# Kernel optimization log

Measured on AMD Instinct MI355X. Metric: run time of the kernel, lower is better.

The kernel has to match this reference:

```python
import jax, jax.numpy as jnp
import numpy as np

H = 4096          # hidden_size
I = 14336         # intermediate_size
SC = int(0.3 * I) # beta * I -> size of cached x_topk (4300)
HC = int(0.05 * I)# gamma * I -> helper top-k count (716)


def setup_inputs() -> dict:
    key = jax.random.key(0)
    ks = jax.random.split(key, 7)
    s = 0.02
    return {
        "x": jax.random.normal(ks[0], (1, 1, H), dtype=jnp.float32),
        "x_topk": jax.random.randint(ks[1], (SC,), 0, I, dtype=jnp.int64),
        "gate_w": jax.random.normal(ks[2], (I, H), dtype=jnp.float32) * s,
        "up_w": jax.random.normal(ks[3], (I, H), dtype=jnp.float32) * s,
        "down_w": jax.random.normal(ks[4], (H, I), dtype=jnp.float32) * s,
        "helper_w1": jax.random.normal(ks[5], (1024, H), dtype=jnp.float32) * s,
        "helper_w2": jax.random.normal(ks[6], (I, 1024), dtype=jnp.float32) * s,
    }


def reference(x, x_topk, gate_w, up_w, down_w, helper_w1, helper_w2):
    # --- sparsity predictor (SimpleLinearModel): two bias-free linears ---
    h = (x @ helper_w1.T) @ helper_w2.T                       # [1,1,I]
    up_mask_index = jax.lax.top_k(h.reshape(-1), HC)[1]       # [HC]

    # --- combine cached core indices with predicted indices, dedup ---
    combined = jnp.concatenate([x_topk.astype(jnp.int32),
                                up_mask_index.astype(jnp.int32)])  # [SC+HC]
    K = combined.shape[0]
    uniq = jnp.unique(combined, size=K, fill_value=I)         # padded with I
    valid = (uniq < I)                                        # [K] bool
    idx = jnp.where(valid, uniq, 0)                           # safe gather idx

    # --- gather weight rows/columns, reduced gated-MLP matmul ---
    gate_f = gate_w[idx]                                      # [K,H]
    up_f = up_w[idx]                                          # [K,H]
    gate_out = jnp.einsum('bsh,kh->bsk', x, gate_f)           # [1,1,K]
    up_out = jnp.einsum('bsh,kh->bsk', x, up_f)               # [1,1,K]
    tv = jax.nn.silu(gate_out) * up_out                       # act_fn = SiLU
    tv = tv * valid.astype(tv.dtype)                          # zero padded dups

    down_f = down_w[:, idx]                                   # [H,K]
    down_value = jnp.einsum('bsk,hk->bsh', tv, down_f)        # [1,1,H]
    return down_value
```

## Files before the change

### kernel.cpp

```cpp
#include <hip/hip_runtime.h>
#include <math.h>

#define H_DIM 4096
#define I_DIM 14336
#define HB_DIM 1024
#define SC_K 4300
#define HC_K 716

__device__ __forceinline__ unsigned sortable(float f) {
    unsigned u = __float_as_uint(f);
    return (u & 0x80000000u) ? ~u : (u | 0x80000000u);
}

__device__ __forceinline__ void compute_tv_row(const float* __restrict__ x,
                                               const float* __restrict__ gate_w,
                                               const float* __restrict__ up_w,
                                               float* __restrict__ tv, int row, int lane) {
    const float* gr = gate_w + (size_t)row * H_DIM;
    const float* ur = up_w + (size_t)row * H_DIM;
    float gs = 0.f, us = 0.f;
#pragma unroll 4
    for (int c = 0; c < H_DIM; c += 256) {
        int cc = c + lane * 4;
        float4 xv = *(const float4*)(x + cc);
        float4 g = *(const float4*)(gr + cc);
        float4 u = *(const float4*)(ur + cc);
        gs += g.x * xv.x + g.y * xv.y + g.z * xv.z + g.w * xv.w;
        us += u.x * xv.x + u.y * xv.y + u.z * xv.z + u.w * xv.w;
    }
#pragma unroll
    for (int o = 32; o >= 1; o >>= 1) {
        gs += __shfl_xor(gs, o);
        us += __shfl_xor(us, o);
    }
    if (lane == 0) {
        float s = gs / (1.f + expf(-gs));
        tv[row] = s * us;
    }
}

__global__ __launch_bounds__(256) void k1_h1_gateup(
    const float* __restrict__ x, const float* __restrict__ hw1,
    const int* __restrict__ x_topk, const float* __restrict__ gate_w,
    const float* __restrict__ up_w, float* __restrict__ h1,
    float* __restrict__ tv) {
    int wid = threadIdx.x >> 6, lane = threadIdx.x & 63;
    int b = blockIdx.x;
    if (b < 256) {
        int row = b * 4 + wid;
        const float* mr = hw1 + (size_t)row * H_DIM;
        float s = 0.f;
#pragma unroll 4
        for (int c = 0; c < H_DIM; c += 256) {
            int cc = c + lane * 4;
            float4 m = *(const float4*)(mr + cc);
            float4 v = *(const float4*)(x + cc);
            s += m.x * v.x + m.y * v.y + m.z * v.z + m.w * v.w;
        }
#pragma unroll
        for (int o = 32; o >= 1; o >>= 1) s += __shfl_xor(s, o);
        if (lane == 0) h1[row] = s;
    } else {
        int gw = (b - 256) * 4 + wid;
        if (gw < SC_K) {
            int idx = x_topk[gw];
            if ((unsigned)idx < (unsigned)I_DIM)
                compute_tv_row(x, gate_w, up_w, tv, idx, lane);
        }
    }
}

__global__ __launch_bounds__(256) void k2_h(
    const float* __restrict__ h1, const float* __restrict__ hw2,
    float* __restrict__ hbuf) {
    int wid = threadIdx.x >> 6, lane = threadIdx.x & 63;
    int row = blockIdx.x * 4 + wid;
    const float* mr = hw2 + (size_t)row * HB_DIM;
    float s = 0.f;
#pragma unroll
    for (int c = 0; c < HB_DIM; c += 256) {
        int cc = c + lane * 4;
        float4 m = *(const float4*)(mr + cc);
        float4 v = *(const float4*)(h1 + cc);
        s += m.x * v.x + m.y * v.y + m.z * v.z + m.w * v.w;
    }
#pragma unroll
    for (int o = 32; o >= 1; o >>= 1) s += __shfl_xor(s, o);
    if (lane == 0) hbuf[row] = s;
}

__global__ __launch_bounds__(1024) void select_kernel(
    const float* __restrict__ h, const int* __restrict__ x_topk,
    float* __restrict__ tv, int* __restrict__ rlist, int* __restrict__ rcount) {
    __shared__ unsigned bins[2048];
    __shared__ unsigned wpart[16];
    __shared__ unsigned bitT[448], bitS[448];
    __shared__ int s_b, s_above, s_tie_cnt, s_rc;
    __shared__ int tie_idx[2048];
    int tid = threadIdx.x;
    int lane = tid & 63, wid = tid >> 6;

    unsigned key[14];
#pragma unroll
    for (int j = 0; j < 14; ++j) key[j] = sortable(h[j * 1024 + tid]);

    if (tid < 448) { bitT[tid] = 0; bitS[tid] = 0; }
    if (tid == 0) { s_tie_cnt = 0; s_rc = 0; }
    __syncthreads();

    for (int k = tid; k < SC_K; k += 1024) {
        int idx = x_topk[k];
        if ((unsigned)idx < (unsigned)I_DIM) atomicOr(&bitT[idx >> 5], 1u << (idx & 31));
    }

    int b1 = 0, b2 = 0;
    int above = 0;
    unsigned T = 0;
    int need2 = 0;

    for (int pass = 0; pass < 3; ++pass) {
        int nb = (pass == 2) ? 1024 : 2048;
        bins[tid] = 0;
        if (nb == 2048) bins[tid + 1024] = 0;
        __syncthreads();
#pragma unroll
        for (int j = 0; j < 14; ++j) {
            unsigned u = key[j];
            bool in_sub = (pass == 0) ||
                          ((pass == 1) ? ((int)(u >> 21) == b1)
                                       : ((int)(u >> 21) == b1 && (int)((u >> 10) & 0x7FF) == b2));
            if (in_sub) {
                unsigned k = (pass == 0) ? (u >> 21)
                           : (pass == 1) ? ((u >> 10) & 0x7FF)
                                         : (u & 0x3FF);
                atomicAdd(&bins[k], 1u);
            }
        }
        __syncthreads();
        unsigned c0 = (2 * tid < nb) ? bins[2 * tid] : 0u;
        unsigned c1 = (2 * tid + 1 < nb) ? bins[2 * tid + 1] : 0u;
        unsigned s = c0 + c1;
        unsigned incl = s;
#pragma unroll
        for (int o = 1; o < 64; o <<= 1) {
            unsigned v = __shfl_up(incl, o);
            if (lane >= o) incl += v;
        }
        if (lane == 63) wpart[wid] = incl;
        __syncthreads();
        if (wid == 0 && lane < 16) {
            unsigned p = wpart[lane];
#pragma unroll
            for (int o = 1; o < 16; o <<= 1) {
                unsigned v = __shfl_up(p, o, 16);
                if (lane >= o) p += v;
            }
            wpart[lane] = p;
        }
        __syncthreads();
        unsigned total = wpart[15];
        unsigned base = (wid > 0 ? wpart[wid - 1] : 0u) + (incl - s);
        unsigned need = (unsigned)(HC_K - above);
        if (2 * tid < nb) {
            unsigned Pm1 = base, P = base + c0;
            if (total - P < need && total - Pm1 >= need) { s_b = 2 * tid; s_above = above + (int)(total - P); }
        }
        if (2 * tid + 1 < nb) {
            unsigned Pm1 = base + c0, P = base + c0 + c1;
            if (total - P < need && total - Pm1 >= need) { s_b = 2 * tid + 1; s_above = above + (int)(total - P); }
        }
        __syncthreads();
        if (pass == 0) b1 = s_b;
        else if (pass == 1) b2 = s_b;
        above = s_above;
        if (pass == 2) {
            T = ((unsigned)b1 << 21) | ((unsigned)b2 << 10) | (unsigned)s_b;
            need2 = HC_K - above;
        }
        __syncthreads();
    }

#pragma unroll
    for (int j = 0; j < 14; ++j) {
        unsigned u = key[j];
        int i = j * 1024 + tid;
        if (u > T) atomicOr(&bitS[i >> 5], 1u << (i & 31));
        else if (u == T) {
            int p = atomicAdd(&s_tie_cnt, 1);
            if (p < 2048) tie_idx[p] = i;
        }
    }
    __syncthreads();
    int C = s_tie_cnt;
    if (C <= 2048) {
        for (int m = tid; m < C; m += 1024) {
            int my = tie_idx[m];
            int rank = 0;
            for (int j = 0; j < C; ++j) rank += (tie_idx[j] < my) ? 1 : 0;
            if (rank < need2) atomicOr(&bitS[my >> 5], 1u << (my & 31));
        }
    } else if (tid == 0) {
        int left = need2;
        for (int i = 0; i < I_DIM && left > 0; ++i)
            if (sortable(h[i]) == T) { atomicOr(&bitS[i >> 5], 1u << (i & 31)); --left; }
    }
    __syncthreads();

#pragma unroll
    for (int j = 0; j < 14; ++j) {
        int i = j * 1024 + tid;
        bool t = (bitT[i >> 5] >> (i & 31)) & 1u;
        bool sl = (bitS[i >> 5] >> (i & 31)) & 1u;
        if (!t) {
            if (sl) {
                int p = atomicAdd(&s_rc, 1);
                rlist[p] = i;
            } else {
                tv[i] = 0.f;
            }
        }
    }
    __syncthreads();
    if (tid == 0) *rcount = s_rc;
}

__global__ __launch_bounds__(256) void k3_residual(
    const float* __restrict__ x, const float* __restrict__ gate_w,
    const float* __restrict__ up_w, const int* __restrict__ rlist,
    const int* __restrict__ rcount, float* __restrict__ tv) {
    int wid = threadIdx.x >> 6, lane = threadIdx.x & 63;
    int gw = blockIdx.x * 4 + wid;
    if (gw < *rcount) compute_tv_row(x, gate_w, up_w, tv, rlist[gw], lane);
}

__global__ __launch_bounds__(256) void k4_down(
    const float* __restrict__ tv, const float* __restrict__ down_w,
    float* __restrict__ out) {
    int wid = threadIdx.x >> 6, lane = threadIdx.x & 63;
    int row = blockIdx.x * 4 + wid;
    const float* mr = down_w + (size_t)row * I_DIM;
    float s = 0.f;
#pragma unroll 4
    for (int c = 0; c < I_DIM; c += 256) {
        int cc = c + lane * 4;
        float4 m = *(const float4*)(mr + cc);
        float4 v = *(const float4*)(tv + cc);
        s += m.x * v.x + m.y * v.y + m.z * v.z + m.w * v.w;
    }
#pragma unroll
    for (int o = 32; o >= 1; o >>= 1) s += __shfl_xor(s, o);
    if (lane == 0) out[row] = s;
}

extern "C" void kernel_launch(void* const* d_in, const int* in_sizes, int n_in,
                              void* d_out, int out_size, void* d_ws, size_t ws_size,
                              hipStream_t stream) {
    const float* x      = (const float*)d_in[0];
    const int*   x_topk = (const int*)d_in[1];
    const float* gate_w = (const float*)d_in[2];
    const float* up_w   = (const float*)d_in[3];
    const float* down_w = (const float*)d_in[4];
    const float* hw1    = (const float*)d_in[5];
    const float* hw2    = (const float*)d_in[6];
    float* out = (float*)d_out;

    float* ws    = (float*)d_ws;
    float* h1    = ws;
    float* hbuf  = ws + 1024;
    float* tv    = ws + 1024 + I_DIM;
    int*   rlist = (int*)(ws + 1024 + 2 * I_DIM);
    int*   rcount = rlist + 768;

    k1_h1_gateup<<<256 + (SC_K + 3) / 4, 256, 0, stream>>>(x, hw1, x_topk, gate_w,
                                                           up_w, h1, tv);
    k2_h<<<I_DIM / 4, 256, 0, stream>>>(h1, hw2, hbuf);
    select_kernel<<<1, 1024, 0, stream>>>(hbuf, x_topk, tv, rlist, rcount);
    k3_residual<<<(HC_K + 3) / 4, 256, 0, stream>>>(x, gate_w, up_w, rlist, rcount, tv);
    k4_down<<<H_DIM / 4, 256, 0, stream>>>(tv, down_w, out);
}
```

Before: 103.7 us.

## Fuse top-k selection with residual gate/up rows, replicating selection per block

The single-block select kernel and the residual gate/up kernel are merged into one kernel launched with 256 blocks. Each block redundantly recomputes the full top-k selection, then handles its own 56-row slice, zeroing unselected tv entries and computing tv for selected rows not already in the cached set. This removes one launch, the rlist/rcount round trip through global memory and the atomic compaction. In exchange every block repeats the radix selection, and the residual rows can be unevenly spread across blocks.

```diff
diff --git a/kernel.cpp b/kernel.cpp
--- a/kernel.cpp
+++ b/kernel.cpp
@@ -89,13 +89,14 @@
     if (lane == 0) hbuf[row] = s;
 }
 
-__global__ __launch_bounds__(1024) void select_kernel(
+__global__ __launch_bounds__(1024) void k3_select_residual(
     const float* __restrict__ h, const int* __restrict__ x_topk,
-    float* __restrict__ tv, int* __restrict__ rlist, int* __restrict__ rcount) {
+    const float* __restrict__ x, const float* __restrict__ gate_w,
+    const float* __restrict__ up_w, float* __restrict__ tv) {
     __shared__ unsigned bins[2048];
     __shared__ unsigned wpart[16];
     __shared__ unsigned bitT[448], bitS[448];
-    __shared__ int s_b, s_above, s_tie_cnt, s_rc;
+    __shared__ int s_b, s_above, s_tie_cnt;
     __shared__ int tie_idx[2048];
     int tid = threadIdx.x;
     int lane = tid & 63, wid = tid >> 6;
@@ -105,7 +106,7 @@
     for (int j = 0; j < 14; ++j) key[j] = sortable(h[j * 1024 + tid]);
 
     if (tid < 448) { bitT[tid] = 0; bitS[tid] = 0; }
-    if (tid == 0) { s_tie_cnt = 0; s_rc = 0; }
+    if (tid == 0) s_tie_cnt = 0;
     __syncthreads();
 
     for (int k = tid; k < SC_K; k += 1024) {
@@ -206,31 +207,19 @@
     }
     __syncthreads();
 
-#pragma unroll
-    for (int j = 0; j < 14; ++j) {
-        int i = j * 1024 + tid;
+    int base_row = blockIdx.x * 56;
+    for (int r = tid; r < 56; r += 1024) {
+        int i = base_row + r;
         bool t = (bitT[i >> 5] >> (i & 31)) & 1u;
         bool sl = (bitS[i >> 5] >> (i & 31)) & 1u;
-        if (!t) {
-            if (sl) {
-                int p = atomicAdd(&s_rc, 1);
-                rlist[p] = i;
-            } else {
-                tv[i] = 0.f;
-            }
-        }
-    }
-    __syncthreads();
-    if (tid == 0) *rcount = s_rc;
-}
-
-__global__ __launch_bounds__(256) void k3_residual(
-    const float* __restrict__ x, const float* __restrict__ gate_w,
-    const float* __restrict__ up_w, const int* __restrict__ rlist,
-    const int* __restrict__ rcount, float* __restrict__ tv) {
-    int wid = threadIdx.x >> 6, lane = threadIdx.x & 63;
-    int gw = blockIdx.x * 4 + wid;
-    if (gw < *rcount) compute_tv_row(x, gate_w, up_w, tv, rlist[gw], lane);
+        if (!t && !sl) tv[i] = 0.f;
+    }
+    for (int r = wid; r < 56; r += 16) {
+        int i = base_row + r;
+        bool t = (bitT[i >> 5] >> (i & 31)) & 1u;
+        bool sl = (bitS[i >> 5] >> (i & 31)) & 1u;
+        if (sl && !t) compute_tv_row(x, gate_w, up_w, tv, i, lane);
+    }
 }
 
 __global__ __launch_bounds__(256) void k4_down(
@@ -264,17 +253,14 @@
     const float* hw2    = (const float*)d_in[6];
     float* out = (float*)d_out;
 
-    float* ws    = (float*)d_ws;
-    float* h1    = ws;
-    float* hbuf  = ws + 1024;
-    float* tv    = ws + 1024 + I_DIM;
-    int*   rlist = (int*)(ws + 1024 + 2 * I_DIM);
-    int*   rcount = rlist + 768;
+    float* ws   = (float*)d_ws;
+    float* h1   = ws;
+    float* hbuf = ws + 1024;
+    float* tv   = ws + 1024 + I_DIM;
 
     k1_h1_gateup<<<256 + (SC_K + 3) / 4, 256, 0, stream>>>(x, hw1, x_topk, gate_w,
                                                            up_w, h1, tv);
     k2_h<<<I_DIM / 4, 256, 0, stream>>>(h1, hw2, hbuf);
-    select_kernel<<<1, 1024, 0, stream>>>(hbuf, x_topk, tv, rlist, rcount);
-    k3_residual<<<(HC_K + 3) / 4, 256, 0, stream>>>(x, gate_w, up_w, rlist, rcount, tv);
+    k3_select_residual<<<256, 1024, 0, stream>>>(hbuf, x_topk, x, gate_w, up_w, tv);
     k4_down<<<H_DIM / 4, 256, 0, stream>>>(tv, down_w, out);
 }
```

Result: slower. 111.5 us (+7.6%).
